# Kernel tuning notes

Hardware: AMD Instinct MI355X
Metric: run time of the kernel (lower is better)

The kernel has to match this reference:

```python
import jax, jax.numpy as jnp
import numpy as np


def _lstm(x, h, c, Wih, Whh, b):
    # torch.nn.LSTMCell gate order: input, forget, cell(g), output
    g = x @ Wih + h @ Whh + b
    i, f, gg, o = jnp.split(g, 4, axis=-1)
    c = jax.nn.sigmoid(f) * c + jax.nn.sigmoid(i) * jnp.tanh(gg)
    h = jax.nn.sigmoid(o) * jnp.tanh(c)
    return h, c


def _forward(memory, mel_target, memory_lengths, prenet_W1, prenet_W2, query_W,
             memory_W, weight_vec, loc_conv_W, loc_dense_W, att_Wih, att_Whh, att_b,
             dec_Wih, dec_Whh, dec_b, proj_W, proj_b, gate_W, gate_b):
    B, n_mels, T_mel = mel_target.shape
    T_enc, enc_dim = memory.shape[1], memory.shape[2]
    att_rnn, dec_rnn = att_Whh.shape[0], dec_Whh.shape[0]
    # decoder inputs: zero frame + teacher-forced mels, one per step -> [T_mel, B, n_mels]
    dec_in = jnp.concatenate(
        [jnp.zeros((1, B, n_mels), memory.dtype), jnp.transpose(mel_target, (2, 0, 1))], 0)[:T_mel]
    # PreNet (dropout disabled: eval mode, torch uses train=self.training)
    pre = jax.nn.relu(jax.nn.relu(dec_in @ prenet_W1) @ prenet_W2)  # [T_mel, B, 256]
    processed_memory = memory @ memory_W                             # [B, T_enc, att_dim]
    valid = jnp.arange(T_enc)[None, :] < memory_lengths[:, None]     # [B, T_enc]
    pad = (loc_conv_W.shape[-1] - 1) // 2

    def step(carry, p):
        ah, ac, dh, dc, aw, awc, ctx = carry
        # attention RNN
        ah, ac = _lstm(jnp.concatenate([p, ctx], -1), ah, ac, att_Wih, att_Whh, att_b)
        # location features: conv over [prev_weights, cum_weights]
        awcat = jnp.stack([aw, awc], 1)                              # [B, 2, T_enc]
        loc = jax.lax.conv_general_dilated(awcat, loc_conv_W, (1,), [(pad, pad)],
                                           dimension_numbers=('NCH', 'OIH', 'NCH'))
        loc = jnp.einsum('bft,fa->bta', loc, loc_dense_W)            # [B, T_enc, att_dim]
        # energies and attention
        q = ah @ query_W                                             # [B, att_dim]
        e = jnp.einsum('bta,a->bt', jnp.tanh(q[:, None, :] + processed_memory + loc), weight_vec)
        e = jnp.where(valid, e, -jnp.inf)
        aw = jax.nn.softmax(e, axis=-1)                              # [B, T_enc]
        ctx = jnp.einsum('bt,btd->bd', aw, memory)                   # [B, enc_dim]
        awc = awc + aw
        # decoder RNN + projections
        dh, dc = _lstm(jnp.concatenate([ah, ctx], -1), dh, dc, dec_Wih, dec_Whh, dec_b)
        do = jnp.concatenate([dh, ctx], -1)
        mel = do @ proj_W + proj_b                                   # [B, n_mels]
        gate = (do @ gate_W + gate_b)[:, 0]                          # [B]
        return (ah, ac, dh, dc, aw, awc, ctx), (mel, gate, aw)

    z = lambda d: jnp.zeros((B, d), memory.dtype)
    carry0 = (z(att_rnn), z(att_rnn), z(dec_rnn), z(dec_rnn),
              jnp.zeros((B, T_enc), memory.dtype), jnp.zeros((B, T_enc), memory.dtype), z(enc_dim))
    _, (mels, gates, aligns) = jax.lax.scan(jax.checkpoint(step), carry0, pre)
    return (jnp.transpose(mels, (1, 2, 0)),   # [B, n_mels, T_mel]
            jnp.transpose(gates, (1, 0)),     # [B, T_mel]
            jnp.transpose(aligns, (1, 0, 2)))  # [B, T_mel, T_enc]


def setup_inputs() -> dict:
    key = jax.random.key(0)
    ks = jax.random.split(key, 20)
    B, T_enc, T_mel = 32, 400, 400
    n_mels, pre, att_rnn, dec_rnn, enc_dim, att_dim, nf, ksz = 80, 256, 1024, 1024, 512, 128, 32, 31
    rn = lambda k, s, sc=0.02: (jax.random.normal(k, s, jnp.float32) * sc)
    return dict(
        memory=jax.random.normal(ks[0], (B, T_enc, enc_dim), jnp.float32),
        mel_target=jax.random.normal(ks[1], (B, n_mels, T_mel), jnp.float32),
        memory_lengths=jax.random.randint(ks[2], (B,), T_enc // 2, T_enc + 1),
        prenet_W1=rn(ks[3], (n_mels, pre), 0.05),
        prenet_W2=rn(ks[4], (pre, pre), 0.05),
        query_W=rn(ks[5], (att_rnn, att_dim)),
        memory_W=rn(ks[6], (enc_dim, att_dim)),
        weight_vec=rn(ks[7], (att_dim,), 0.1),
        loc_conv_W=rn(ks[8], (nf, 2, ksz), 0.1),
        loc_dense_W=rn(ks[9], (nf, att_dim), 0.1),
        att_Wih=rn(ks[10], (pre + enc_dim, 4 * att_rnn)),
        att_Whh=rn(ks[11], (att_rnn, 4 * att_rnn)),
        att_b=jnp.zeros((4 * att_rnn,), jnp.float32),
        dec_Wih=rn(ks[12], (att_rnn + enc_dim, 4 * dec_rnn)),
        dec_Whh=rn(ks[13], (dec_rnn, 4 * dec_rnn)),
        dec_b=jnp.zeros((4 * dec_rnn,), jnp.float32),
        proj_W=rn(ks[14], (dec_rnn + enc_dim, n_mels)),
        proj_b=jnp.zeros((n_mels,), jnp.float32),
        gate_W=rn(ks[15], (dec_rnn + enc_dim, 1)),
        gate_b=jnp.zeros((1,), jnp.float32),
    )


def reference(memory, mel_target, memory_lengths, prenet_W1, prenet_W2, query_W,
              memory_W, weight_vec, loc_conv_W, loc_dense_W, att_Wih, att_Whh, att_b,
              dec_Wih, dec_Whh, dec_b, proj_W, proj_b, gate_W, gate_b):
    return _forward(memory, mel_target, memory_lengths, prenet_W1, prenet_W2, query_W,
                    memory_W, weight_vec, loc_conv_W, loc_dense_W, att_Wih, att_Whh, att_b,
                    dec_Wih, dec_Whh, dec_b, proj_W, proj_b, gate_W, gate_b)
```

## Files before the change

kernel.cpp:

```cpp
#include <hip/hip_runtime.h>

#define OFF_PRE   0u
#define OFF_PMT   3276800u
#define OFF_GATT  4915200u
#define OFF_GDEC  5963776u
#define OFF_E     8060928u
#define OFF_AH    8073728u
#define OFF_AC0   8106496u
#define OFF_AC1   8139264u
#define OFF_DH    8172032u
#define OFF_DC    8204800u
#define OFF_AW0   8237568u
#define OFF_AW1   8250368u
#define OFF_AWC0  8263168u
#define OFF_AWC1  8275968u
#define OFF_CTX0  8288768u
#define OFF_CTX1  8305152u
#define WS_TOTAL  8321536u

__device__ __forceinline__ float sigm(float x){ return 1.f/(1.f+__expf(-x)); }
__device__ __forceinline__ float ftanh(float x){
  x = fminf(fmaxf(x,-15.f),15.f);
  float e = __expf(2.f*x);
  return (e-1.f)/(e+1.f);
}


__global__ void zero_kernel(float* p, unsigned n){
  unsigned i = blockIdx.x*256u + threadIdx.x;
  if (i<n) p[i]=0.f;
}

__global__ __launch_bounds__(256) void prenet_kernel(const float* __restrict__ mel_target,
    const float* __restrict__ W1, const float* __restrict__ W2, float* __restrict__ pre)
{
  __shared__ float din[80];
  __shared__ float h1[256];
  int blk = blockIdx.x;
  int t = blk >> 5, b = blk & 31;
  int tid = threadIdx.x;
  if (tid < 80) din[tid] = (t==0) ? 0.f : mel_target[b*32000 + tid*400 + (t-1)];
  __syncthreads();
  float s=0.f;
  for (int c=0;c<80;c++) s += din[c]*W1[c*256+tid];
  h1[tid] = fmaxf(s,0.f);
  __syncthreads();
  float s2=0.f;
  for (int c=0;c<256;c++) s2 += h1[c]*W2[c*256+tid];
  pre[(size_t)blk*256 + tid] = fmaxf(s2,0.f);
}

__global__ __launch_bounds__(128) void pm_kernel(const float* __restrict__ memory,
    const float* __restrict__ memory_W, float* __restrict__ pmT)
{
  __shared__ float mrow[512];
  int blk = blockIdx.x;
  int b = blk/400, t = blk - b*400;
  int tid = threadIdx.x;
  const float* src = memory + (size_t)blk*512;
  for (int i=tid;i<512;i+=128) mrow[i]=src[i];
  __syncthreads();
  float s=0.f;
  for (int d=0; d<512; d++) s += mrow[d]*memory_W[d*128+tid];
  pmT[(size_t)b*51200 + tid*400 + t] = s;
}

template<int SLICE, int KIH>
__global__ __launch_bounds__(512) void gates_kernel(
    const float* __restrict__ x0, int n0,
    const float* __restrict__ x1, int n1,
    const float* __restrict__ x2, int n2,
    const float* __restrict__ Wih, const float* __restrict__ Whh,
    float* __restrict__ Gp)
{
  __shared__ float xs[SLICE*33];
  const int tid = threadIdx.x;
  const int k_beg = blockIdx.y * SLICE;
  const int k_end = k_beg + SLICE;
  const int n01 = n0 + n1;
  for (int base=0; base<32*SLICE; base+=512){
    int idx = base + tid;
    if (idx < 32*SLICE){
      int r = idx / SLICE, kk = idx - r*SLICE;
      int k = k_beg + kk;
      float v;
      if (k < n0) v = x0[r*n0 + k];
      else if (k < n01) v = x1[r*n1 + (k-n0)];
      else v = x2[r*n2 + (k-n01)];
      xs[kk*33 + r] = v;
    }
  }
  __syncthreads();
  const int rg = tid >> 5, cg = tid & 31;
  const int r0 = rg*2;
  const int colb = blockIdx.x*128 + cg*4;
  float4 a0 = {0,0,0,0}, a1 = {0,0,0,0};
  const int kA = (k_end < KIH) ? k_end : KIH;
  const int kB = (k_beg > KIH) ? k_beg : KIH;
  #pragma unroll 4
  for (int k=k_beg; k<kA; k++){
    float4 w = *(const float4*)(Wih + (size_t)k*4096 + colb);
    int kk = k - k_beg;
    float xv0 = xs[kk*33 + r0], xv1 = xs[kk*33 + r0 + 1];
    a0.x += xv0*w.x; a0.y += xv0*w.y; a0.z += xv0*w.z; a0.w += xv0*w.w;
    a1.x += xv1*w.x; a1.y += xv1*w.y; a1.z += xv1*w.z; a1.w += xv1*w.w;
  }
  #pragma unroll 4
  for (int k=kB; k<k_end; k++){
    float4 w = *(const float4*)(Whh + (size_t)(k-KIH)*4096 + colb);
    int kk = k - k_beg;
    float xv0 = xs[kk*33 + r0], xv1 = xs[kk*33 + r0 + 1];
    a0.x += xv0*w.x; a0.y += xv0*w.y; a0.z += xv0*w.z; a0.w += xv0*w.w;
    a1.x += xv1*w.x; a1.y += xv1*w.y; a1.z += xv1*w.z; a1.w += xv1*w.w;
  }
  float* gp = Gp + (size_t)blockIdx.y*131072 + colb;
  *(float4*)(gp + (size_t)(r0  )*4096) = a0;
  *(float4*)(gp + (size_t)(r0+1)*4096) = a1;
}

__global__ __launch_bounds__(512) void att_mid_kernel(
    const float* __restrict__ Gp, const float* __restrict__ att_b,
    float* __restrict__ AH, const float* __restrict__ ACr, float* __restrict__ ACw,
    const float* __restrict__ query_W,
    const float* __restrict__ wc, const float* __restrict__ wd,
    const float* __restrict__ vvec, const float* __restrict__ pmT,
    const int* __restrict__ mlen,
    const float* __restrict__ AWr, const float* __restrict__ AWCr,
    float* __restrict__ E,
    const float* __restrict__ Gd, const float* __restrict__ dec_b,
    float* __restrict__ DH, float* __restrict__ DC,
    int step)
{
  __shared__ float aw_s[400], awc_s[400];
  __shared__ float wc_s[1984];
  __shared__ float wd_s[4096];
  __shared__ float v_s[128], q_s[128];
  __shared__ float ah_s[1024];
  __shared__ float pool[4608];
  const int b = blockIdx.x, yD = blockIdx.y, tid = threadIdx.x;

  for (int i=tid;i<400;i+=512){ aw_s[i]=AWr[b*400+i]; awc_s[i]=AWCr[b*400+i]; }
  for (int i=tid;i<4096;i+=512) wd_s[i]=wd[i];
  for (int i=tid;i<1984;i+=512) wc_s[i]=wc[i];
  if (tid<128) v_s[tid]=vvec[tid];

  {
    float4* g4 = (float4*)pool;
    for (int i=tid; i<1024; i+=512){
      float4 s = {0,0,0,0};
      #pragma unroll
      for (int sl=0; sl<8; sl++){
        const float4* gs = (const float4*)(Gp + (size_t)sl*131072 + (size_t)b*4096);
        float4 v = gs[i];
        s.x+=v.x; s.y+=v.y; s.z+=v.z; s.w+=v.w;
      }
      g4[i] = s;
    }
  }
  __syncthreads();
  for (int u0=0; u0<2; u0++){
    int u = tid + u0*512;
    float gi=pool[u]+att_b[u], gf=pool[1024+u]+att_b[1024+u];
    float gg=pool[2048+u]+att_b[2048+u], go=pool[3072+u]+att_b[3072+u];
    float c = sigm(gf)*ACr[b*1024+u] + sigm(gi)*ftanh(gg);
    float h = sigm(go)*ftanh(c);
    ah_s[u]=h;
    if (yD==0){ ACw[b*1024+u]=c; AH[b*1024+u]=h; }
  }
  __syncthreads();
  { int a = tid & 127, sl = tid >> 7;
    float s=0.f; int kb = sl*256;
    for (int k=kb;k<kb+256;k++) s += ah_s[k]*query_W[k*128+a];
    pool[sl*128+a]=s; }
  __syncthreads();
  if (tid<128) q_s[tid] = pool[tid]+pool[128+tid]+pool[256+tid]+pool[384+tid];
  if (step>0 && tid<128){
    int u = yD*128 + tid;
    float gi=dec_b[u], gf=dec_b[1024+u], gg=dec_b[2048+u], go=dec_b[3072+u];
    #pragma unroll
    for (int sl=0; sl<16; sl++){
      const float* g = Gd + (size_t)sl*131072 + (size_t)b*4096;
      gi+=g[u]; gf+=g[1024+u]; gg+=g[2048+u]; go+=g[3072+u];
    }
    float c = sigm(gf)*DC[b*1024+u] + sigm(gi)*ftanh(gg);
    float h = sigm(go)*ftanh(c);
    DC[b*1024+u]=c; DH[b*1024+u]=h;
  }
  __syncthreads();
  const int t0 = yD*50;
  float* loc = pool + 512;
  { int tl = tid & 63, fs = tid >> 6;
    if (tl < 50){
      float cf0=0,cf1=0,cf2=0,cf3=0;
      int f0 = fs*4;
      int tg = t0 + tl;
      for (int k=0;k<31;k++){
        int gi2 = tg + k - 15;
        float a1 = (gi2>=0 && gi2<400) ? aw_s[gi2] : 0.f;
        float a2 = (gi2>=0 && gi2<400) ? awc_s[gi2] : 0.f;
        cf0 += wc_s[(f0+0)*62+k]*a1 + wc_s[(f0+0)*62+31+k]*a2;
        cf1 += wc_s[(f0+1)*62+k]*a1 + wc_s[(f0+1)*62+31+k]*a2;
        cf2 += wc_s[(f0+2)*62+k]*a1 + wc_s[(f0+2)*62+31+k]*a2;
        cf3 += wc_s[(f0+3)*62+k]*a1 + wc_s[(f0+3)*62+31+k]*a2;
      }
      loc[tl*33+f0+0]=cf0; loc[tl*33+f0+1]=cf1;
      loc[tl*33+f0+2]=cf2; loc[tl*33+f0+3]=cf3;
    }
  }
  __syncthreads();
  float* ep = pool + 2176;
  { int tl = tid & 63, as = tid >> 6;
    if (tl < 50){
      int tg = t0 + tl;
      float e = 0.f;
      const float* lrow = loc + tl*33;
      for (int aa=0; aa<16; aa++){
        int a = as*16 + aa;
        float pmv = pmT[(size_t)b*51200 + (size_t)a*400 + tg];
        float lv = 0.f;
        #pragma unroll
        for (int f=0; f<32; f++) lv += lrow[f]*wd_s[f*128+a];
        e += ftanh(q_s[a]+pmv+lv)*v_s[a];
      }
      ep[as*64+tl] = e;
    }
  }
  __syncthreads();
  if (tid < 50){
    int tg = t0 + tid;
    float ee=0.f;
    #pragma unroll
    for (int as2=0; as2<8; as2++) ee += ep[as2*64+tid];
    E[b*400+tg] = (tg < mlen[b]) ? ee : -1e30f;
  }
}

__global__ __launch_bounds__(512) void softmax_ctx_kernel(
    const float* __restrict__ E, const float* __restrict__ memory,
    float* __restrict__ AWw, const float* __restrict__ AWCr, float* __restrict__ AWCw,
    float* __restrict__ CTXw, const float* __restrict__ CTXpp,
    const float* __restrict__ DH,
    const float* __restrict__ proj_W, const float* __restrict__ proj_b,
    const float* __restrict__ gate_W, const float* __restrict__ gate_b,
    float* __restrict__ out, float* __restrict__ aligns, int step)
{
  __shared__ float e_s[400];
  __shared__ float red[16];
  __shared__ float cp[512];
  __shared__ float do_s[1536];
  __shared__ float pps[486];
  const int b = blockIdx.x, yD = blockIdx.y, tid = threadIdx.x;

  float ev = (tid<400) ? E[b*400+tid] : -1e30f;
  float m = ev;
  for (int off=32; off>0; off>>=1) m = fmaxf(m, __shfl_down(m, off, 64));
  if ((tid&63)==0) red[tid>>6]=m;
  __syncthreads();
  if (tid==0){ float mm=red[0]; for (int i=1;i<8;i++) mm=fmaxf(mm,red[i]); red[8]=mm; }
  __syncthreads();
  m = red[8];
  float ex = (tid<400) ? __expf(ev-m) : 0.f;
  float ss = ex;
  for (int off=32; off>0; off>>=1) ss += __shfl_down(ss, off, 64);
  if ((tid&63)==0) red[tid>>6]=ss;
  __syncthreads();
  if (tid==0){ float s2=0.f; for (int i=0;i<8;i++) s2+=red[i]; red[9]=1.f/s2; }
  __syncthreads();
  float anew = ex*red[9];
  if (tid<400) e_s[tid]=anew;
  if (yD==0 && tid<400){
    AWw[b*400+tid] = anew;
    AWCw[b*400+tid] = AWCr[b*400+tid] + anew;
    aligns[(size_t)b*160000 + (size_t)step*400 + tid] = anew;
  }
  __syncthreads();
  { int d = tid & 63, ts = tid >> 6;
    const int d0 = yD*64;
    const float* mrow = memory + (size_t)b*204800 + d0 + d;
    float pacc=0.f;
    for (int tt=ts*50; tt<ts*50+50; tt++) pacc += e_s[tt]*mrow[(size_t)tt*512];
    cp[ts*64+d]=pacc; }
  __syncthreads();
  if (tid<64){
    float s2=0.f;
    #pragma unroll
    for (int ts2=0; ts2<8; ts2++) s2+=cp[ts2*64+tid];
    CTXw[b*512 + yD*64 + tid]=s2;
  }
  if (yD==0 && step>0){
    for (int i=tid; i<1536; i+=512)
      do_s[i] = (i<1024) ? DH[b*1024+i] : CTXpp[b*512 + (i-1024)];
    __syncthreads();
    int sl = tid/81, o = tid - sl*81;
    if (sl < 6){
      float s=0.f; int kb = sl*256;
      for (int k=kb;k<kb+256;k++){
        float w2 = (o<80) ? proj_W[k*80+o] : gate_W[k];
        s += do_s[k]*w2;
      }
      pps[sl*81+o]=s;
    }
    __syncthreads();
    if (tid<81){
      float r=0.f;
      #pragma unroll
      for (int s2=0;s2<6;s2++) r += pps[s2*81+tid];
      if (tid<80) out[(size_t)b*32000 + tid*400 + (step-1)] = r + proj_b[tid];
      else        out[1024000 + b*400 + (step-1)] = r + gate_b[0];
    }
  }
}

__global__ __launch_bounds__(512) void dec_final_kernel(
    const float* __restrict__ Gd, const float* __restrict__ dec_b,
    const float* __restrict__ DC, const float* __restrict__ CTX1,
    const float* __restrict__ proj_W, const float* __restrict__ proj_b,
    const float* __restrict__ gate_W, const float* __restrict__ gate_b,
    float* __restrict__ out)
{
  __shared__ float g_s[4096];
  __shared__ float do_s[1536];
  __shared__ float pps[486];
  const int b = blockIdx.x, tid = threadIdx.x;
  { float4* g4 = (float4*)g_s;
    for (int i=tid; i<1024; i+=512){
      float4 s={0,0,0,0};
      #pragma unroll
      for (int sl=0; sl<16; sl++){
        const float4* gs = (const float4*)(Gd + (size_t)sl*131072 + (size_t)b*4096);
        float4 v = gs[i];
        s.x+=v.x; s.y+=v.y; s.z+=v.z; s.w+=v.w;
      }
      g4[i]=s;
    } }
  __syncthreads();
  for (int u0=0; u0<2; u0++){
    int u = tid + u0*512;
    float gi=g_s[u]+dec_b[u], gf=g_s[1024+u]+dec_b[1024+u];
    float gg=g_s[2048+u]+dec_b[2048+u], go=g_s[3072+u]+dec_b[3072+u];
    float c = sigm(gf)*DC[b*1024+u] + sigm(gi)*ftanh(gg);
    do_s[u] = sigm(go)*ftanh(c);
  }
  if (tid<512) do_s[1024+tid] = CTX1[b*512+tid];
  __syncthreads();
  int sl = tid/81, o = tid - sl*81;
  if (sl < 6){
    float s=0.f; int kb = sl*256;
    for (int k=kb;k<kb+256;k++){
      float w2 = (o<80) ? proj_W[k*80+o] : gate_W[k];
      s += do_s[k]*w2;
    }
    pps[sl*81+o]=s;
  }
  __syncthreads();
  if (tid<81){
    float r=0.f;
    #pragma unroll
    for (int s2=0;s2<6;s2++) r += pps[s2*81+tid];
    if (tid<80) out[(size_t)b*32000 + tid*400 + 399] = r + proj_b[tid];
    else        out[1024000 + b*400 + 399] = r + gate_b[0];
  }
}


extern "C" void kernel_launch(void* const* d_in, const int* in_sizes, int n_in,
                              void* d_out, int out_size, void* d_ws, size_t ws_size,
                              hipStream_t stream) {
  const float* memory      = (const float*)d_in[0];
  const float* mel_target  = (const float*)d_in[1];
  const int*   mlen        = (const int*)  d_in[2];
  const float* prenet_W1   = (const float*)d_in[3];
  const float* prenet_W2   = (const float*)d_in[4];
  const float* query_W     = (const float*)d_in[5];
  const float* memory_W    = (const float*)d_in[6];
  const float* weight_vec  = (const float*)d_in[7];
  const float* loc_conv_W  = (const float*)d_in[8];
  const float* loc_dense_W = (const float*)d_in[9];
  const float* att_Wih     = (const float*)d_in[10];
  const float* att_Whh     = (const float*)d_in[11];
  const float* att_b       = (const float*)d_in[12];
  const float* dec_Wih     = (const float*)d_in[13];
  const float* dec_Whh     = (const float*)d_in[14];
  const float* dec_b       = (const float*)d_in[15];
  const float* proj_W      = (const float*)d_in[16];
  const float* proj_b      = (const float*)d_in[17];
  const float* gate_W      = (const float*)d_in[18];
  const float* gate_b      = (const float*)d_in[19];
  float* out = (float*)d_out;
  float* ws  = (float*)d_ws;

  float* PRE  = ws + OFF_PRE;
  float* PMT  = ws + OFF_PMT;
  float* GATT = ws + OFF_GATT;
  float* GDEC = ws + OFF_GDEC;
  float* E    = ws + OFF_E;
  float* AH   = ws + OFF_AH;
  float* AC[2] = { ws + OFF_AC0, ws + OFF_AC1 };
  float* DH   = ws + OFF_DH;
  float* DC   = ws + OFF_DC;
  float* AW[2] = { ws + OFF_AW0, ws + OFF_AW1 };
  float* AWC[2]= { ws + OFF_AWC0, ws + OFF_AWC1 };
  float* CTX[2]= { ws + OFF_CTX0, ws + OFF_CTX1 };
  float* aligns = out + 1036800;

  hipLaunchKernelGGL(zero_kernel, dim3((WS_TOTAL+255u)/256u), dim3(256), 0, stream, ws, WS_TOTAL);
  hipLaunchKernelGGL(prenet_kernel, dim3(12800), dim3(256), 0, stream,
                     mel_target, prenet_W1, prenet_W2, PRE);
  hipLaunchKernelGGL(pm_kernel, dim3(12800), dim3(128), 0, stream, memory, memory_W, PMT);

  for (int t=0; t<400; t++){
    const int p = t & 1, pp = 1 - p;
    hipLaunchKernelGGL((gates_kernel<224,768>), dim3(32,8), dim3(512), 0, stream,
        PRE + (size_t)t*8192, 256, CTX[pp], 512, AH, 1024,
        att_Wih, att_Whh, GATT);
    hipLaunchKernelGGL(att_mid_kernel, dim3(32,8), dim3(512), 0, stream,
        GATT, att_b, AH, AC[pp], AC[p], query_W, loc_conv_W, loc_dense_W,
        weight_vec, PMT, mlen, AW[pp], AWC[pp], E,
        GDEC, dec_b, DH, DC, t);
    hipLaunchKernelGGL(softmax_ctx_kernel, dim3(32,8), dim3(512), 0, stream,
        E, memory, AW[p], AWC[pp], AWC[p], CTX[p], CTX[pp],
        DH, proj_W, proj_b, gate_W, gate_b, out, aligns, t);
    hipLaunchKernelGGL((gates_kernel<160,1536>), dim3(32,16), dim3(512), 0, stream,
        AH, 1024, CTX[p], 512, DH, 1024,
        dec_Wih, dec_Whh, GDEC);
  }
  hipLaunchKernelGGL(dec_final_kernel, dim3(32), dim3(512), 0, stream,
      GDEC, dec_b, DC, CTX[1], proj_W, proj_b, gate_W, gate_b, out);
}
```

Before: 80.38 ms.

## Stream gate weights through LDS with async triple-buffered global_load_lds

The LSTM gate GEMV kernel now stages weight tiles of 16 rows into a triple-buffered LDS ring using the direct global-to-LDS load builtin. Waits are placed with explicit vmcnt and barriers so loads for later tiles overlap the FMAs on the current tile. The attention-gates launch also uses half the K-slice and twice the grid in y, with the workspace and the partial-sum reduction widened to 16 slices. This aims to hide weight-streaming latency and raise parallelism, at the cost of more partial sums to reduce and extra barriers per tile.

```diff
diff --git a/kernel.cpp b/kernel.cpp
--- a/kernel.cpp
+++ b/kernel.cpp
@@ -3,20 +3,20 @@
 #define OFF_PRE   0u
 #define OFF_PMT   3276800u
 #define OFF_GATT  4915200u
-#define OFF_GDEC  5963776u
-#define OFF_E     8060928u
-#define OFF_AH    8073728u
-#define OFF_AC0   8106496u
-#define OFF_AC1   8139264u
-#define OFF_DH    8172032u
-#define OFF_DC    8204800u
-#define OFF_AW0   8237568u
-#define OFF_AW1   8250368u
-#define OFF_AWC0  8263168u
-#define OFF_AWC1  8275968u
-#define OFF_CTX0  8288768u
-#define OFF_CTX1  8305152u
-#define WS_TOTAL  8321536u
+#define OFF_GDEC  7012352u
+#define OFF_E     9109504u
+#define OFF_AH    9122304u
+#define OFF_AC0   9155072u
+#define OFF_AC1   9187840u
+#define OFF_DH    9220608u
+#define OFF_DC    9253376u
+#define OFF_AW0   9286144u
+#define OFF_AW1   9298944u
+#define OFF_AWC0  9311744u
+#define OFF_AWC1  9324544u
+#define OFF_CTX0  9337344u
+#define OFF_CTX1  9353728u
+#define WS_TOTAL  9370112u
 
 __device__ __forceinline__ float sigm(float x){ return 1.f/(1.f+__expf(-x)); }
 __device__ __forceinline__ float ftanh(float x){
@@ -24,6 +24,9 @@
   float e = __expf(2.f*x);
   return (e-1.f)/(e+1.f);
 }
+
+typedef const __attribute__((address_space(1))) unsigned int* gas_t;
+typedef __attribute__((address_space(3))) unsigned int* las_t;
 
 
 __global__ void zero_kernel(float* p, unsigned n){
@@ -66,18 +69,20 @@
 }
 
 template<int SLICE, int KIH>
-__global__ __launch_bounds__(512) void gates_kernel(
+__global__ __launch_bounds__(512) void gates_v3(
     const float* __restrict__ x0, int n0,
     const float* __restrict__ x1, int n1,
     const float* __restrict__ x2, int n2,
     const float* __restrict__ Wih, const float* __restrict__ Whh,
     float* __restrict__ Gp)
 {
+  constexpr int NT = SLICE/16;
   __shared__ float xs[SLICE*33];
+  __shared__ float wbuf[3*2048];
   const int tid = threadIdx.x;
   const int k_beg = blockIdx.y * SLICE;
-  const int k_end = k_beg + SLICE;
   const int n01 = n0 + n1;
+
   for (int base=0; base<32*SLICE; base+=512){
     int idx = base + tid;
     if (idx < 32*SLICE){
@@ -91,29 +96,48 @@
     }
   }
   __syncthreads();
+
+  const int wv = tid >> 6, lane = tid & 63;
+  const int fb = wv*1024 + lane*16;
+  const int kk_l = fb >> 9;
+  const int inner = fb & 511;
+  const size_t colbB = (size_t)blockIdx.x*512;
+
+  auto STAGE = [&](int s){
+    int k = k_beg + s*16 + kk_l;
+    const char* row = (k < KIH) ? ((const char*)Wih + (size_t)k*16384)
+                                : ((const char*)Whh + (size_t)(k-KIH)*16384);
+    const char* g = row + colbB + inner;
+    float* l = &wbuf[(s%3)*2048 + wv*256];
+    __builtin_amdgcn_global_load_lds((gas_t)g, (las_t)l, 16, 0, 0);
+  };
+
+  STAGE(0);
+  STAGE(1);
+
   const int rg = tid >> 5, cg = tid & 31;
   const int r0 = rg*2;
-  const int colb = blockIdx.x*128 + cg*4;
   float4 a0 = {0,0,0,0}, a1 = {0,0,0,0};
-  const int kA = (k_end < KIH) ? k_end : KIH;
-  const int kB = (k_beg > KIH) ? k_beg : KIH;
-  #pragma unroll 4
-  for (int k=k_beg; k<kA; k++){
-    float4 w = *(const float4*)(Wih + (size_t)k*4096 + colb);
-    int kk = k - k_beg;
-    float xv0 = xs[kk*33 + r0], xv1 = xs[kk*33 + r0 + 1];
-    a0.x += xv0*w.x; a0.y += xv0*w.y; a0.z += xv0*w.z; a0.w += xv0*w.w;
-    a1.x += xv1*w.x; a1.y += xv1*w.y; a1.z += xv1*w.z; a1.w += xv1*w.w;
-  }
-  #pragma unroll 4
-  for (int k=kB; k<k_end; k++){
-    float4 w = *(const float4*)(Whh + (size_t)(k-KIH)*4096 + colb);
-    int kk = k - k_beg;
-    float xv0 = xs[kk*33 + r0], xv1 = xs[kk*33 + r0 + 1];
-    a0.x += xv0*w.x; a0.y += xv0*w.y; a0.z += xv0*w.z; a0.w += xv0*w.w;
-    a1.x += xv1*w.x; a1.y += xv1*w.y; a1.z += xv1*w.z; a1.w += xv1*w.w;
-  }
-  float* gp = Gp + (size_t)blockIdx.y*131072 + colb;
+
+  for (int s=0; s<NT; s++){
+    asm volatile("s_barrier" ::: "memory");
+    if (s+2 < NT) STAGE(s+2);
+    int rem = NT-1-s;
+    if (rem >= 2)      asm volatile("s_waitcnt vmcnt(2)" ::: "memory");
+    else if (rem == 1) asm volatile("s_waitcnt vmcnt(1)" ::: "memory");
+    else               asm volatile("s_waitcnt vmcnt(0)" ::: "memory");
+    asm volatile("s_barrier" ::: "memory");
+    const float* wb = &wbuf[(s%3)*2048];
+    const float* xk = &xs[(s*16)*33];
+    #pragma unroll
+    for (int kk=0; kk<16; kk++){
+      float4 w = *(const float4*)(wb + kk*128 + cg*4);
+      float xv0 = xk[kk*33 + r0], xv1 = xk[kk*33 + r0 + 1];
+      a0.x += xv0*w.x; a0.y += xv0*w.y; a0.z += xv0*w.z; a0.w += xv0*w.w;
+      a1.x += xv1*w.x; a1.y += xv1*w.y; a1.z += xv1*w.z; a1.w += xv1*w.w;
+    }
+  }
+  float* gp = Gp + (size_t)blockIdx.y*131072 + blockIdx.x*128 + cg*4;
   *(float4*)(gp + (size_t)(r0  )*4096) = a0;
   *(float4*)(gp + (size_t)(r0+1)*4096) = a1;
 }
@@ -149,7 +173,7 @@
     for (int i=tid; i<1024; i+=512){
       float4 s = {0,0,0,0};
       #pragma unroll
-      for (int sl=0; sl<8; sl++){
+      for (int sl=0; sl<16; sl++){
         const float4* gs = (const float4*)(Gp + (size_t)sl*131072 + (size_t)b*4096);
         float4 v = gs[i];
         s.x+=v.x; s.y+=v.y; s.z+=v.z; s.w+=v.w;
@@ -410,7 +434,7 @@
 
   for (int t=0; t<400; t++){
     const int p = t & 1, pp = 1 - p;
-    hipLaunchKernelGGL((gates_kernel<224,768>), dim3(32,8), dim3(512), 0, stream,
+    hipLaunchKernelGGL((gates_v3<112,768>), dim3(32,16), dim3(512), 0, stream,
         PRE + (size_t)t*8192, 256, CTX[pp], 512, AH, 1024,
         att_Wih, att_Whh, GATT);
     hipLaunchKernelGGL(att_mid_kernel, dim3(32,8), dim3(512), 0, stream,
@@ -420,7 +444,7 @@
     hipLaunchKernelGGL(softmax_ctx_kernel, dim3(32,8), dim3(512), 0, stream,
         E, memory, AW[p], AWC[pp], AWC[p], CTX[p], CTX[pp],
         DH, proj_W, proj_b, gate_W, gate_b, out, aligns, t);
-    hipLaunchKernelGGL((gates_kernel<160,1536>), dim3(32,16), dim3(512), 0, stream,
+    hipLaunchKernelGGL((gates_v3<160,1536>), dim3(32,16), dim3(512), 0, stream,
         AH, 1024, CTX[p], 512, DH, 1024,
         dec_Wih, dec_Whh, GDEC);
   }
```

After: 71.90 ms. 10.6% less time.
